# Performance work log

Measured on AMD Instinct MI355X. Metric: run time of the kernel, lower is better.

Reference implementation:

```python
import jax, jax.numpy as jnp
import numpy as np

B, H, I, E = 4096, 1024, 4096, 8
TOP_K = 2


def setup_inputs() -> dict:
    key = jax.random.key(0)
    ks = jax.random.split(key, 8)
    s = 0.02
    return {
        "x": jax.random.normal(ks[0], (B, H), jnp.float32),
        "noise": -jnp.log(-jnp.log(jax.random.uniform(ks[1], (B, E), jnp.float32) + 1e-20) + 1e-20),
        "Wr": jax.random.normal(ks[2], (H, E), jnp.float32) * s,
        "br": jnp.zeros((E,), jnp.float32),
        "W_in": jax.random.normal(ks[3], (E, H, 2 * I), jnp.float32) * s,
        "b_in": jnp.zeros((E, 2 * I), jnp.float32),
        "W_out": jax.random.normal(ks[4], (E, I, H), jnp.float32) * s,
        "b_out": jnp.zeros((E, H), jnp.float32),
    }


def reference(x, noise, Wr, br, W_in, b_in, W_out, b_out):
    # Router + Gumbel top-2 (temperature = 1.0)
    logits = x @ Wr + br                      # [B, E]
    y = logits + noise
    vals, idxs = jax.lax.top_k(y, TOP_K)      # [B, 2]
    w = jax.nn.softmax(vals, axis=-1)         # softmax over the 2 selected vals
    # Dense gate matrix: gates[b, e] = sum_k w[b,k] * (idxs[b,k] == e)
    onehot = (idxs[:, :, None] == jnp.arange(E)[None, None, :]).astype(x.dtype)  # [B,2,E]
    gates = jnp.einsum("bk,bke->be", w, onehot)                                   # [B,E]

    out = jnp.zeros_like(x)
    for e in range(E):  # small static expert loop
        h = x @ W_in[e] + b_in[e]             # [B, 2I]
        x1, x2 = jnp.split(h, 2, axis=-1)     # SwiGLU: chunk(2, dim=-1)
        a = x1 * jax.nn.sigmoid(x2)           # [B, I]
        o = a @ W_out[e] + b_out[e]           # [B, H]
        out = out + gates[:, e:e + 1] * o
    # dropout is identity in eval mode
    return out
```

## Files before the change

kernel.cpp:

```cpp
#include <hip/hip_runtime.h>

#define B_TOK 4096
#define HDIM 1024
#define IDIM 4096
#define NSLOT 8192
#define MAX_T128 72

using short8   = __attribute__((ext_vector_type(8))) short;
using bf16x8   = __attribute__((ext_vector_type(8))) __bf16;
using f32x4    = __attribute__((ext_vector_type(4))) float;
using int4v    = __attribute__((ext_vector_type(4))) int;
using ushort4v = __attribute__((ext_vector_type(4))) unsigned short;
using float4v  = __attribute__((ext_vector_type(4))) float;

#define MC_NT128   0
#define MC_E128    8
#define MC_M0128   80
#define MC_RW128   152
#define META_INTS  256

__device__ __forceinline__ unsigned short f2bf(float f) {
  unsigned u = __float_as_uint(f);
  u += 0x7FFFu + ((u >> 16) & 1u);
  return (unsigned short)(u >> 16);
}
__device__ __forceinline__ float bf2f(unsigned short h) {
  return __uint_as_float(((unsigned)h) << 16);
}
__device__ __forceinline__ f32x4 mfma_bf16(short8 a, short8 b, f32x4 c) {
  return __builtin_amdgcn_mfma_f32_16x16x32_bf16(
      __builtin_bit_cast(bf16x8, a), __builtin_bit_cast(bf16x8, b), c, 0, 0, 0);
}
__device__ __forceinline__ void gload16(const unsigned short* g, unsigned short* l) {
  __builtin_amdgcn_global_load_lds(
      (const __attribute__((address_space(1))) unsigned int*)g,
      (__attribute__((address_space(3))) unsigned int*)l, 16, 0, 0);
}

__global__ __launch_bounds__(256) void router_kernel(
    const float* __restrict__ x, const float* __restrict__ noise,
    const float* __restrict__ Wr, const float* __restrict__ br,
    int* __restrict__ idxmap, float* __restrict__ wmap) {
  int tok = blockIdx.x * 4 + (threadIdx.x >> 6);
  int l = threadIdx.x & 63;
  const float* xr = x + (size_t)tok * HDIM;
  float acc[8];
#pragma unroll
  for (int e = 0; e < 8; e++) acc[e] = 0.f;
  for (int hb = 0; hb < HDIM; hb += 256) {
    int h = hb + l * 4;
    float4v xv = *(const float4v*)(xr + h);
#pragma unroll
    for (int j = 0; j < 4; j++) {
      float4v w0 = *(const float4v*)(Wr + (size_t)(h + j) * 8);
      float4v w1 = *(const float4v*)(Wr + (size_t)(h + j) * 8 + 4);
      acc[0] += xv[j] * w0[0]; acc[1] += xv[j] * w0[1];
      acc[2] += xv[j] * w0[2]; acc[3] += xv[j] * w0[3];
      acc[4] += xv[j] * w1[0]; acc[5] += xv[j] * w1[1];
      acc[6] += xv[j] * w1[2]; acc[7] += xv[j] * w1[3];
    }
  }
#pragma unroll
  for (int off = 32; off > 0; off >>= 1) {
#pragma unroll
    for (int e = 0; e < 8; e++) acc[e] += __shfl_xor(acc[e], off, 64);
  }
  if (l == 0) {
    float y[8];
#pragma unroll
    for (int e = 0; e < 8; e++) y[e] = acc[e] + br[e] + noise[(size_t)tok * 8 + e];
    int e0 = 0;
#pragma unroll
    for (int e = 1; e < 8; e++) if (y[e] > y[e0]) e0 = e;
    int e1 = (e0 == 0) ? 1 : 0;
#pragma unroll
    for (int e = 0; e < 8; e++) if (e != e0 && y[e] > y[e1]) e1 = e;
    float w0 = 1.f / (1.f + __expf(y[e1] - y[e0]));
    idxmap[tok * 2] = e0; idxmap[tok * 2 + 1] = e1;
    wmap[tok * 2] = w0;   wmap[tok * 2 + 1] = 1.f - w0;
  }
}

__global__ __launch_bounds__(1024) void rank_kernel(
    const int* __restrict__ idxmap, int* __restrict__ slotmap,
    int* __restrict__ meta) {
  int tid = threadIdx.x, lane = tid & 63, wv = tid >> 6;
  __shared__ unsigned wtot[16][4];
  __shared__ unsigned woff[16][4];
  __shared__ unsigned offE[8];

  int es[8];
  unsigned p0 = 0, p1 = 0, p2 = 0, p3 = 0;
#pragma unroll
  for (int j = 0; j < 8; j++) {
    int e = idxmap[tid * 8 + j];
    es[j] = e;
    unsigned c = 1u << ((e & 1) * 16);
    if (e < 2) p0 += c; else if (e < 4) p1 += c;
    else if (e < 6) p2 += c; else p3 += c;
  }
  unsigned i0 = p0, i1 = p1, i2 = p2, i3 = p3;
#pragma unroll
  for (int d = 1; d < 64; d <<= 1) {
    unsigned t0 = __shfl_up(i0, d, 64), t1 = __shfl_up(i1, d, 64);
    unsigned t2 = __shfl_up(i2, d, 64), t3 = __shfl_up(i3, d, 64);
    if (lane >= d) { i0 += t0; i1 += t1; i2 += t2; i3 += t3; }
  }
  if (lane == 63) { wtot[wv][0] = i0; wtot[wv][1] = i1; wtot[wv][2] = i2; wtot[wv][3] = i3; }
  __syncthreads();
  if (wv == 0 && lane < 16) {
    unsigned a0 = wtot[lane][0], a1 = wtot[lane][1], a2 = wtot[lane][2], a3 = wtot[lane][3];
    unsigned s0 = a0, s1 = a1, s2 = a2, s3 = a3;
#pragma unroll
    for (int d = 1; d < 16; d <<= 1) {
      unsigned t0 = __shfl_up(s0, d, 64), t1 = __shfl_up(s1, d, 64);
      unsigned t2 = __shfl_up(s2, d, 64), t3 = __shfl_up(s3, d, 64);
      if (lane >= d) { s0 += t0; s1 += t1; s2 += t2; s3 += t3; }
    }
    woff[lane][0] = s0 - a0; woff[lane][1] = s1 - a1;
    woff[lane][2] = s2 - a2; woff[lane][3] = s3 - a3;
    if (lane == 15) {
      unsigned t[8];
      t[0] = s0 & 0xFFFF; t[1] = s0 >> 16; t[2] = s1 & 0xFFFF; t[3] = s1 >> 16;
      t[4] = s2 & 0xFFFF; t[5] = s2 >> 16; t[6] = s3 & 0xFFFF; t[7] = s3 >> 16;
      unsigned off = 0; int tc = 0;
      for (int e = 0; e < 8; e++) {
        offE[e] = off;
        for (unsigned i = 0; i < t[e]; i += 128) {
          meta[MC_E128 + tc] = e;
          meta[MC_M0128 + tc] = (int)(off + i);
          meta[MC_RW128 + tc] = (int)((t[e] - i < 128u) ? (t[e] - i) : 128u);
          tc++;
        }
        off += t[e];
      }
      meta[MC_NT128] = tc;
    }
  }
  __syncthreads();
  unsigned e0w = i0 - p0 + woff[wv][0];
  unsigned e1w = i1 - p1 + woff[wv][1];
  unsigned e2w = i2 - p2 + woff[wv][2];
  unsigned e3w = i3 - p3 + woff[wv][3];
#pragma unroll
  for (int j = 0; j < 8; j++) {
    int e = es[j];
    unsigned sh = (unsigned)(e & 1) * 16;
    unsigned c = 1u << sh, v;
    if (e < 2)      { v = (e0w >> sh) & 0xFFFF; e0w += c; }
    else if (e < 4) { v = (e1w >> sh) & 0xFFFF; e1w += c; }
    else if (e < 6) { v = (e2w >> sh) & 0xFFFF; e2w += c; }
    else            { v = (e3w >> sh) & 0xFFFF; e3w += c; }
    slotmap[tid * 8 + j] = (int)(offE[e] + v);
  }
}

__global__ __launch_bounds__(256) void place_kernel(
    const float* __restrict__ x, const int* __restrict__ slotmap,
    unsigned short* __restrict__ x_g) {
  int tok = blockIdx.x * 2 + (threadIdx.x >> 7);
  int h = (threadIdx.x & 127) * 8;
  const float* xr = x + (size_t)tok * HDIM + h;
  float4v v0 = *(const float4v*)xr;
  float4v v1 = *(const float4v*)(xr + 4);
  int4v p;
  p[0] = (int)((unsigned)f2bf(v0[0]) | ((unsigned)f2bf(v0[1]) << 16));
  p[1] = (int)((unsigned)f2bf(v0[2]) | ((unsigned)f2bf(v0[3]) << 16));
  p[2] = (int)((unsigned)f2bf(v1[0]) | ((unsigned)f2bf(v1[1]) << 16));
  p[3] = (int)((unsigned)f2bf(v1[2]) | ((unsigned)f2bf(v1[3]) << 16));
  int s0 = slotmap[tok * 2], s1 = slotmap[tok * 2 + 1];
  *(int4v*)(x_g + (size_t)s0 * HDIM + h) = p;
  *(int4v*)(x_g + (size_t)s1 * HDIM + h) = p;
}

__global__ __launch_bounds__(256) void prep_win_kernel(
    const float* __restrict__ W_in, unsigned short* __restrict__ Wt) {
  int e = blockIdx.z, k0 = blockIdx.y * 64, n0 = blockIdx.x * 64;
  __shared__ __align__(16) unsigned short T[64 * 72];
  int tid = threadIdx.x;
#pragma unroll
  for (int i = 0; i < 4; i++) {
    int q = i * 256 + tid;
    int kr = q >> 4, nc = (q & 15) * 4;
    float4v v = *(const float4v*)(W_in + ((size_t)e * 1024 + k0 + kr) * 8192 + n0 + nc);
#pragma unroll
    for (int j = 0; j < 4; j++) T[(nc + j) * 72 + kr] = f2bf(v[j]);
  }
  __syncthreads();
  int half = (n0 >= 4096) ? 1 : 0;
  int j0 = n0 - half * 4096;
  int J = j0 >> 6;
  unsigned short* ob = Wt + (((size_t)e * 64 + J) << 17);
#pragma unroll
  for (int i = 0; i < 2; i++) {
    int q = i * 256 + tid;
    int nr = q >> 3, kc = (q & 7) * 8;
    int pr = (nr >> 4) * 32 + half * 16 + (nr & 15);
    *(int4v*)(ob + (size_t)pr * 1024 + k0 + kc) = *(const int4v*)&T[nr * 72 + kc];
  }
}

__global__ __launch_bounds__(256) void prep_wout_kernel(
    const float* __restrict__ W_out, unsigned short* __restrict__ Wt) {
  int e = blockIdx.z, k0 = blockIdx.y * 64, n0 = blockIdx.x * 64;
  __shared__ __align__(16) unsigned short T[64 * 72];
  int tid = threadIdx.x;
#pragma unroll
  for (int i = 0; i < 4; i++) {
    int q = i * 256 + tid;
    int kr = q >> 4, nc = (q & 15) * 4;
    float4v v = *(const float4v*)(W_out + ((size_t)e * 4096 + k0 + kr) * 1024 + n0 + nc);
#pragma unroll
    for (int j = 0; j < 4; j++) T[(nc + j) * 72 + kr] = f2bf(v[j]);
  }
  __syncthreads();
  unsigned short* ob = Wt + ((size_t)e * 1024 + n0) * 4096;
#pragma unroll
  for (int i = 0; i < 2; i++) {
    int q = i * 256 + tid;
    int nr = q >> 3, kc = (q & 7) * 8;
    *(int4v*)(ob + (size_t)nr * 4096 + k0 + kc) = *(const int4v*)&T[nr * 72 + kc];
  }
}

__global__ __launch_bounds__(256, 4) void gemm1a_kernel(
    const unsigned short* __restrict__ x_g, const unsigned short* __restrict__ Wt,
    const float* __restrict__ b_in, unsigned short* __restrict__ a_buf,
    const int* __restrict__ meta) {
  int bid = blockIdx.x;
  int xcd = bid & 7, local = bid >> 3;
  int t = local >> 3;
  if (t >= meta[MC_NT128]) return;
  int J = xcd * 8 + (local & 7);
  int e = meta[MC_E128 + t];
  int m0 = meta[MC_M0128 + t];
  int rows = meta[MC_RW128 + t];
  const unsigned short* Wp = Wt + (((size_t)e * 64 + J) << 17);

  __shared__ __align__(16) unsigned short As[128 * 64];
  __shared__ __align__(16) unsigned short Bs[128 * 64];

  int tid = threadIdx.x, l = tid & 63, w = tid >> 6;
  int g = l >> 4, ln = l & 15, lr = l >> 3;
  int uc = (l & 7) ^ lr;
  int wm = w >> 1, wn = w & 1;

  const unsigned short* sA[4]; const unsigned short* sB[4]; int dO[4];
#pragma unroll
  for (int i = 0; i < 4; i++) {
    int c = w * 4 + i;
    int r = c * 8 + lr;
    int ra = r < rows ? r : rows - 1;
    sA[i] = x_g + (size_t)(m0 + ra) * HDIM + uc * 8;
    sB[i] = Wp + (size_t)r * 1024 + uc * 8;
    dO[i] = c * 512 + l * 8;
  }

  f32x4 acc[4][4];
#pragma unroll
  for (int mf = 0; mf < 4; mf++)
#pragma unroll
    for (int nf = 0; nf < 4; nf++) acc[mf][nf] = (f32x4){0.f, 0.f, 0.f, 0.f};

#pragma unroll 1
  for (int kt = 0; kt < 16; kt++) {
#pragma unroll
    for (int i = 0; i < 4; i++) gload16(sA[i] + kt * 64, &As[dO[i]]);
#pragma unroll
    for (int i = 0; i < 4; i++) gload16(sB[i] + kt * 64, &Bs[dO[i]]);
    __syncthreads();
#pragma unroll
    for (int ks = 0; ks < 2; ks++) {
      int u0 = (((ks * 4 + g) ^ (ln & 7)) << 3);
      short8 af[4], bfr[4];
#pragma unroll
      for (int mf = 0; mf < 4; mf++)
        af[mf] = *(const short8*)&As[(wm * 64 + mf * 16 + ln) * 64 + u0];
#pragma unroll
      for (int nf = 0; nf < 4; nf++)
        bfr[nf] = *(const short8*)&Bs[(wn * 64 + nf * 16 + ln) * 64 + u0];
#pragma unroll
      for (int mf = 0; mf < 4; mf++)
#pragma unroll
        for (int nf = 0; nf < 4; nf++)
          acc[mf][nf] = mfma_bf16(af[mf], bfr[nf], acc[mf][nf]);
    }
    __syncthreads();
  }
#pragma unroll
  for (int mf = 0; mf < 4; mf++) {
#pragma unroll
    for (int np = 0; np < 2; np++) {
      int j = J * 64 + wn * 32 + np * 16 + ln;
      float b1 = b_in[(size_t)e * 8192 + j];
      float b2 = b_in[(size_t)e * 8192 + 4096 + j];
#pragma unroll
      for (int r = 0; r < 4; r++) {
        int m = wm * 64 + mf * 16 + g * 4 + r;
        if (m < rows) {
          float h1 = acc[mf][np * 2][r] + b1;
          float h2 = acc[mf][np * 2 + 1][r] + b2;
          a_buf[(size_t)(m0 + m) * IDIM + j] = f2bf(h1 / (1.f + __expf(-h2)));
        }
      }
    }
  }
}

__global__ __launch_bounds__(256, 4) void gemm2a_kernel(
    const unsigned short* __restrict__ a_buf, const unsigned short* __restrict__ Wt,
    const float* __restrict__ b_out, unsigned short* __restrict__ buf2,
    const int* __restrict__ meta) {
  int bid = blockIdx.x;
  int xcd = bid & 7, local = bid >> 3;
  int t = local >> 1;
  if (t >= meta[MC_NT128]) return;
  int n0 = xcd * 128 + (local & 1) * 64;
  int e = meta[MC_E128 + t];
  int m0 = meta[MC_M0128 + t];
  int rows = meta[MC_RW128 + t];
  const unsigned short* Wp = Wt + ((size_t)e * 1024 + n0) * 4096;

  __shared__ __align__(16) unsigned short As[128 * 64];
  __shared__ __align__(16) unsigned short Bs[64 * 64];

  int tid = threadIdx.x, l = tid & 63, w = tid >> 6;
  int g = l >> 4, ln = l & 15, lr = l >> 3;
  int uc = (l & 7) ^ lr;
  int wm = w >> 1, wn = w & 1;

  const unsigned short* sA[4]; int dAo[4];
#pragma unroll
  for (int i = 0; i < 4; i++) {
    int c = w * 4 + i;
    int r = c * 8 + lr;
    int ra = r < rows ? r : rows - 1;
    sA[i] = a_buf + (size_t)(m0 + ra) * IDIM + uc * 8;
    dAo[i] = c * 512 + l * 8;
  }
  const unsigned short* sB[2]; int dBo[2];
#pragma unroll
  for (int i = 0; i < 2; i++) {
    int c = w * 2 + i;
    int r = c * 8 + lr;
    sB[i] = Wp + (size_t)r * 4096 + uc * 8;
    dBo[i] = c * 512 + l * 8;
  }

  f32x4 acc[4][2];
#pragma unroll
  for (int mf = 0; mf < 4; mf++)
#pragma unroll
    for (int nf = 0; nf < 2; nf++) acc[mf][nf] = (f32x4){0.f, 0.f, 0.f, 0.f};

#pragma unroll 1
  for (int kt = 0; kt < 64; kt++) {
#pragma unroll
    for (int i = 0; i < 4; i++) gload16(sA[i] + kt * 64, &As[dAo[i]]);
#pragma unroll
    for (int i = 0; i < 2; i++) gload16(sB[i] + kt * 64, &Bs[dBo[i]]);
    __syncthreads();
#pragma unroll
    for (int ks = 0; ks < 2; ks++) {
      int u0 = (((ks * 4 + g) ^ (ln & 7)) << 3);
      short8 af[4], bfr[2];
#pragma unroll
      for (int mf = 0; mf < 4; mf++)
        af[mf] = *(const short8*)&As[(wm * 64 + mf * 16 + ln) * 64 + u0];
#pragma unroll
      for (int nf = 0; nf < 2; nf++)
        bfr[nf] = *(const short8*)&Bs[(wn * 32 + nf * 16 + ln) * 64 + u0];
#pragma unroll
      for (int mf = 0; mf < 4; mf++)
#pragma unroll
        for (int nf = 0; nf < 2; nf++)
          acc[mf][nf] = mfma_bf16(af[mf], bfr[nf], acc[mf][nf]);
    }
    __syncthreads();
  }
#pragma unroll
  for (int mf = 0; mf < 4; mf++) {
#pragma unroll
    for (int nf = 0; nf < 2; nf++) {
      int col = n0 + wn * 32 + nf * 16 + ln;
      float bo = b_out[(size_t)e * 1024 + col];
#pragma unroll
      for (int r = 0; r < 4; r++) {
        int m = wm * 64 + mf * 16 + g * 4 + r;
        if (m < rows) {
          buf2[(size_t)(m0 + m) * HDIM + col] = f2bf(acc[mf][nf][r] + bo);
        }
      }
    }
  }
}

__global__ __launch_bounds__(256) void combine_kernel(
    const unsigned short* __restrict__ buf2, const int* __restrict__ slotmap,
    const float* __restrict__ wmap, float* __restrict__ out) {
  int i = blockIdx.x * 256 + threadIdx.x;
  int base = i * 4;
  int b = base >> 10, h = base & 1023;
  int s0 = slotmap[b * 2], s1 = slotmap[b * 2 + 1];
  float w0 = wmap[b * 2], w1 = wmap[b * 2 + 1];
  ushort4v c0 = *(const ushort4v*)(buf2 + (size_t)s0 * HDIM + h);
  ushort4v c1 = *(const ushort4v*)(buf2 + (size_t)s1 * HDIM + h);
  float4v o;
#pragma unroll
  for (int j = 0; j < 4; j++) o[j] = w0 * bf2f(c0[j]) + w1 * bf2f(c1[j]);
  *(float4v*)(out + base) = o;
}

extern "C" void kernel_launch(void* const* d_in, const int* in_sizes, int n_in,
                              void* d_out, int out_size, void* d_ws, size_t ws_size,
                              hipStream_t stream) {
  const float* x     = (const float*)d_in[0];
  const float* noise = (const float*)d_in[1];
  const float* Wr    = (const float*)d_in[2];
  const float* br    = (const float*)d_in[3];
  const float* W_in  = (const float*)d_in[4];
  const float* b_in  = (const float*)d_in[5];
  const float* W_out = (const float*)d_in[6];
  const float* b_out = (const float*)d_in[7];
  float* out = (float*)d_out;
  char* ws = (char*)d_ws;

  unsigned short* W_in_t  = (unsigned short*)ws;
  unsigned short* W_out_t = W_in_t;
  unsigned short* x_g     = (unsigned short*)(ws + 134217728);
  unsigned short* buf2    = x_g;
  unsigned short* a_buf   = (unsigned short*)(ws + 150994944);
  int* meta    = (int*)(ws + 218103808);
  int* idxmap  = meta + META_INTS;
  int* slotmap = idxmap + NSLOT;
  float* wmap  = (float*)(slotmap + NSLOT);

  hipLaunchKernelGGL(router_kernel, dim3(B_TOK / 4), dim3(256), 0, stream,
                     x, noise, Wr, br, idxmap, wmap);
  hipLaunchKernelGGL(rank_kernel, dim3(1), dim3(1024), 0, stream,
                     idxmap, slotmap, meta);
  hipLaunchKernelGGL(place_kernel, dim3(B_TOK / 2), dim3(256), 0, stream,
                     x, slotmap, x_g);
  hipLaunchKernelGGL(prep_win_kernel, dim3(128, 16, 8), dim3(256), 0, stream,
                     W_in, W_in_t);
  hipLaunchKernelGGL(gemm1a_kernel, dim3(8 * MAX_T128 * 8), dim3(256), 0, stream,
                     x_g, W_in_t, b_in, a_buf, meta);
  hipLaunchKernelGGL(prep_wout_kernel, dim3(16, 64, 8), dim3(256), 0, stream,
                     W_out, W_out_t);
  hipLaunchKernelGGL(gemm2a_kernel, dim3(8 * MAX_T128 * 2), dim3(256), 0, stream,
                     a_buf, W_out_t, b_out, buf2, meta);
  hipLaunchKernelGGL(combine_kernel, dim3((B_TOK * HDIM / 4) / 256), dim3(256), 0, stream,
                     buf2, slotmap, wmap, out);
}
```

Before: 451.1 us.

## Fuse weight prep into router and gemm1 launches, widen gemm2 N-tile

```diff
diff --git a/kernel.cpp b/kernel.cpp
--- a/kernel.cpp
+++ b/kernel.cpp
@@ -5,6 +5,7 @@
 #define IDIM 4096
 #define NSLOT 8192
 #define MAX_T128 72
+#define G1_BLOCKS (8 * MAX_T128 * 8)
 
 using short8   = __attribute__((ext_vector_type(8))) short;
 using bf16x8   = __attribute__((ext_vector_type(8))) __bf16;
@@ -37,47 +38,99 @@
       (__attribute__((address_space(3))) unsigned int*)l, 16, 0, 0);
 }
 
-__global__ __launch_bounds__(256) void router_kernel(
+__device__ __forceinline__ void prep_wout_body(
+    const float* __restrict__ W_out, unsigned short* __restrict__ Wt,
+    int bx, int by, int e, unsigned short* T, int tid) {
+  int k0 = by * 64, n0 = bx * 64;
+#pragma unroll
+  for (int i = 0; i < 4; i++) {
+    int q = i * 256 + tid;
+    int kr = q >> 4, nc = (q & 15) * 4;
+    float4v v = *(const float4v*)(W_out + ((size_t)e * 4096 + k0 + kr) * 1024 + n0 + nc);
+#pragma unroll
+    for (int j = 0; j < 4; j++) T[(nc + j) * 72 + kr] = f2bf(v[j]);
+  }
+  __syncthreads();
+  unsigned short* ob = Wt + ((size_t)e * 1024 + n0) * 4096;
+#pragma unroll
+  for (int i = 0; i < 2; i++) {
+    int q = i * 256 + tid;
+    int nr = q >> 3, kc = (q & 7) * 8;
+    *(int4v*)(ob + (size_t)nr * 4096 + k0 + kc) = *(const int4v*)&T[nr * 72 + kc];
+  }
+}
+
+__global__ __launch_bounds__(256) void fused_pre_kernel(
     const float* __restrict__ x, const float* __restrict__ noise,
     const float* __restrict__ Wr, const float* __restrict__ br,
-    int* __restrict__ idxmap, float* __restrict__ wmap) {
-  int tok = blockIdx.x * 4 + (threadIdx.x >> 6);
-  int l = threadIdx.x & 63;
-  const float* xr = x + (size_t)tok * HDIM;
-  float acc[8];
-#pragma unroll
-  for (int e = 0; e < 8; e++) acc[e] = 0.f;
-  for (int hb = 0; hb < HDIM; hb += 256) {
-    int h = hb + l * 4;
-    float4v xv = *(const float4v*)(xr + h);
-#pragma unroll
-    for (int j = 0; j < 4; j++) {
-      float4v w0 = *(const float4v*)(Wr + (size_t)(h + j) * 8);
-      float4v w1 = *(const float4v*)(Wr + (size_t)(h + j) * 8 + 4);
-      acc[0] += xv[j] * w0[0]; acc[1] += xv[j] * w0[1];
-      acc[2] += xv[j] * w0[2]; acc[3] += xv[j] * w0[3];
-      acc[4] += xv[j] * w1[0]; acc[5] += xv[j] * w1[1];
-      acc[6] += xv[j] * w1[2]; acc[7] += xv[j] * w1[3];
-    }
-  }
-#pragma unroll
-  for (int off = 32; off > 0; off >>= 1) {
-#pragma unroll
-    for (int e = 0; e < 8; e++) acc[e] += __shfl_xor(acc[e], off, 64);
-  }
-  if (l == 0) {
-    float y[8];
-#pragma unroll
-    for (int e = 0; e < 8; e++) y[e] = acc[e] + br[e] + noise[(size_t)tok * 8 + e];
-    int e0 = 0;
-#pragma unroll
-    for (int e = 1; e < 8; e++) if (y[e] > y[e0]) e0 = e;
-    int e1 = (e0 == 0) ? 1 : 0;
-#pragma unroll
-    for (int e = 0; e < 8; e++) if (e != e0 && y[e] > y[e1]) e1 = e;
-    float w0 = 1.f / (1.f + __expf(y[e1] - y[e0]));
-    idxmap[tok * 2] = e0; idxmap[tok * 2 + 1] = e1;
-    wmap[tok * 2] = w0;   wmap[tok * 2 + 1] = 1.f - w0;
+    int* __restrict__ idxmap, float* __restrict__ wmap,
+    const float* __restrict__ W_in, unsigned short* __restrict__ Wt) {
+  __shared__ __align__(16) unsigned short T[64 * 72];
+  int bid = blockIdx.x;
+  int tid = threadIdx.x;
+  if (bid < 1024) {
+    int tok = bid * 4 + (tid >> 6);
+    int l = tid & 63;
+    const float* xr = x + (size_t)tok * HDIM;
+    float acc[8];
+#pragma unroll
+    for (int e = 0; e < 8; e++) acc[e] = 0.f;
+    for (int hb = 0; hb < HDIM; hb += 256) {
+      int h = hb + l * 4;
+      float4v xv = *(const float4v*)(xr + h);
+#pragma unroll
+      for (int j = 0; j < 4; j++) {
+        float4v w0 = *(const float4v*)(Wr + (size_t)(h + j) * 8);
+        float4v w1 = *(const float4v*)(Wr + (size_t)(h + j) * 8 + 4);
+        acc[0] += xv[j] * w0[0]; acc[1] += xv[j] * w0[1];
+        acc[2] += xv[j] * w0[2]; acc[3] += xv[j] * w0[3];
+        acc[4] += xv[j] * w1[0]; acc[5] += xv[j] * w1[1];
+        acc[6] += xv[j] * w1[2]; acc[7] += xv[j] * w1[3];
+      }
+    }
+#pragma unroll
+    for (int off = 32; off > 0; off >>= 1) {
+#pragma unroll
+      for (int e = 0; e < 8; e++) acc[e] += __shfl_xor(acc[e], off, 64);
+    }
+    if (l == 0) {
+      float y[8];
+#pragma unroll
+      for (int e = 0; e < 8; e++) y[e] = acc[e] + br[e] + noise[(size_t)tok * 8 + e];
+      int e0 = 0;
+#pragma unroll
+      for (int e = 1; e < 8; e++) if (y[e] > y[e0]) e0 = e;
+      int e1 = (e0 == 0) ? 1 : 0;
+#pragma unroll
+      for (int e = 0; e < 8; e++) if (e != e0 && y[e] > y[e1]) e1 = e;
+      float w0 = 1.f / (1.f + __expf(y[e1] - y[e0]));
+      idxmap[tok * 2] = e0; idxmap[tok * 2 + 1] = e1;
+      wmap[tok * 2] = w0;   wmap[tok * 2 + 1] = 1.f - w0;
+    }
+    return;
+  }
+  int pid = bid - 1024;
+  int e = pid >> 11, rem = pid & 2047;
+  int k0 = (rem >> 7) * 64, n0 = (rem & 127) * 64;
+#pragma unroll
+  for (int i = 0; i < 4; i++) {
+    int q = i * 256 + tid;
+    int kr = q >> 4, nc = (q & 15) * 4;
+    float4v v = *(const float4v*)(W_in + ((size_t)e * 1024 + k0 + kr) * 8192 + n0 + nc);
+#pragma unroll
+    for (int j = 0; j < 4; j++) T[(nc + j) * 72 + kr] = f2bf(v[j]);
+  }
+  __syncthreads();
+  int half = (n0 >= 4096) ? 1 : 0;
+  int j0 = n0 - half * 4096;
+  int J = j0 >> 6;
+  unsigned short* ob = Wt + (((size_t)e * 64 + J) << 17);
+#pragma unroll
+  for (int i = 0; i < 2; i++) {
+    int q = i * 256 + tid;
+    int nr = q >> 3, kc = (q & 7) * 8;
+    int pr = (nr >> 4) * 32 + half * 16 + (nr & 15);
+    *(int4v*)(ob + (size_t)pr * 1024 + k0 + kc) = *(const int4v*)&T[nr * 72 + kc];
   }
 }
 
@@ -173,61 +226,26 @@
   *(int4v*)(x_g + (size_t)s1 * HDIM + h) = p;
 }
 
-__global__ __launch_bounds__(256) void prep_win_kernel(
-    const float* __restrict__ W_in, unsigned short* __restrict__ Wt) {
-  int e = blockIdx.z, k0 = blockIdx.y * 64, n0 = blockIdx.x * 64;
-  __shared__ __align__(16) unsigned short T[64 * 72];
-  int tid = threadIdx.x;
-#pragma unroll
-  for (int i = 0; i < 4; i++) {
-    int q = i * 256 + tid;
-    int kr = q >> 4, nc = (q & 15) * 4;
-    float4v v = *(const float4v*)(W_in + ((size_t)e * 1024 + k0 + kr) * 8192 + n0 + nc);
-#pragma unroll
-    for (int j = 0; j < 4; j++) T[(nc + j) * 72 + kr] = f2bf(v[j]);
-  }
-  __syncthreads();
-  int half = (n0 >= 4096) ? 1 : 0;
-  int j0 = n0 - half * 4096;
-  int J = j0 >> 6;
-  unsigned short* ob = Wt + (((size_t)e * 64 + J) << 17);
-#pragma unroll
-  for (int i = 0; i < 2; i++) {
-    int q = i * 256 + tid;
-    int nr = q >> 3, kc = (q & 7) * 8;
-    int pr = (nr >> 4) * 32 + half * 16 + (nr & 15);
-    *(int4v*)(ob + (size_t)pr * 1024 + k0 + kc) = *(const int4v*)&T[nr * 72 + kc];
-  }
-}
-
 __global__ __launch_bounds__(256) void prep_wout_kernel(
     const float* __restrict__ W_out, unsigned short* __restrict__ Wt) {
-  int e = blockIdx.z, k0 = blockIdx.y * 64, n0 = blockIdx.x * 64;
   __shared__ __align__(16) unsigned short T[64 * 72];
-  int tid = threadIdx.x;
-#pragma unroll
-  for (int i = 0; i < 4; i++) {
-    int q = i * 256 + tid;
-    int kr = q >> 4, nc = (q & 15) * 4;
-    float4v v = *(const float4v*)(W_out + ((size_t)e * 4096 + k0 + kr) * 1024 + n0 + nc);
-#pragma unroll
-    for (int j = 0; j < 4; j++) T[(nc + j) * 72 + kr] = f2bf(v[j]);
-  }
-  __syncthreads();
-  unsigned short* ob = Wt + ((size_t)e * 1024 + n0) * 4096;
-#pragma unroll
-  for (int i = 0; i < 2; i++) {
-    int q = i * 256 + tid;
-    int nr = q >> 3, kc = (q & 7) * 8;
-    *(int4v*)(ob + (size_t)nr * 4096 + k0 + kc) = *(const int4v*)&T[nr * 72 + kc];
-  }
+  prep_wout_body(W_out, Wt, blockIdx.x, blockIdx.y, blockIdx.z, T, threadIdx.x);
 }
 
 __global__ __launch_bounds__(256, 4) void gemm1a_kernel(
     const unsigned short* __restrict__ x_g, const unsigned short* __restrict__ Wt,
     const float* __restrict__ b_in, unsigned short* __restrict__ a_buf,
-    const int* __restrict__ meta) {
+    const int* __restrict__ meta,
+    const float* __restrict__ W_out, unsigned short* __restrict__ Wot) {
+  __shared__ __align__(16) unsigned short As[128 * 64];
+  __shared__ __align__(16) unsigned short Bs[128 * 64];
   int bid = blockIdx.x;
+  if (bid >= G1_BLOCKS) {
+    int pid = bid - G1_BLOCKS;
+    int e = pid >> 10, rem = pid & 1023;
+    prep_wout_body(W_out, Wot, rem & 15, rem >> 4, e, As, threadIdx.x);
+    return;
+  }
   int xcd = bid & 7, local = bid >> 3;
   int t = local >> 3;
   if (t >= meta[MC_NT128]) return;
@@ -237,9 +255,6 @@
   int rows = meta[MC_RW128 + t];
   const unsigned short* Wp = Wt + (((size_t)e * 64 + J) << 17);
 
-  __shared__ __align__(16) unsigned short As[128 * 64];
-  __shared__ __align__(16) unsigned short Bs[128 * 64];
-
   int tid = threadIdx.x, l = tid & 63, w = tid >> 6;
   int g = l >> 4, ln = l & 15, lr = l >> 3;
   int uc = (l & 7) ^ lr;
@@ -312,68 +327,61 @@
     const float* __restrict__ b_out, unsigned short* __restrict__ buf2,
     const int* __restrict__ meta) {
   int bid = blockIdx.x;
-  int xcd = bid & 7, local = bid >> 3;
-  int t = local >> 1;
+  int xcd = bid & 7;
+  int t = bid >> 3;
   if (t >= meta[MC_NT128]) return;
-  int n0 = xcd * 128 + (local & 1) * 64;
+  int n0 = xcd * 128;
   int e = meta[MC_E128 + t];
   int m0 = meta[MC_M0128 + t];
   int rows = meta[MC_RW128 + t];
   const unsigned short* Wp = Wt + ((size_t)e * 1024 + n0) * 4096;
 
   __shared__ __align__(16) unsigned short As[128 * 64];
-  __shared__ __align__(16) unsigned short Bs[64 * 64];
+  __shared__ __align__(16) unsigned short Bs[128 * 64];
 
   int tid = threadIdx.x, l = tid & 63, w = tid >> 6;
   int g = l >> 4, ln = l & 15, lr = l >> 3;
   int uc = (l & 7) ^ lr;
   int wm = w >> 1, wn = w & 1;
 
-  const unsigned short* sA[4]; int dAo[4];
+  const unsigned short* sA[4]; const unsigned short* sB[4]; int dO[4];
 #pragma unroll
   for (int i = 0; i < 4; i++) {
     int c = w * 4 + i;
     int r = c * 8 + lr;
     int ra = r < rows ? r : rows - 1;
     sA[i] = a_buf + (size_t)(m0 + ra) * IDIM + uc * 8;
-    dAo[i] = c * 512 + l * 8;
-  }
-  const unsigned short* sB[2]; int dBo[2];
-#pragma unroll
-  for (int i = 0; i < 2; i++) {
-    int c = w * 2 + i;
-    int r = c * 8 + lr;
     sB[i] = Wp + (size_t)r * 4096 + uc * 8;
-    dBo[i] = c * 512 + l * 8;
-  }
-
-  f32x4 acc[4][2];
+    dO[i] = c * 512 + l * 8;
+  }
+
+  f32x4 acc[4][4];
 #pragma unroll
   for (int mf = 0; mf < 4; mf++)
 #pragma unroll
-    for (int nf = 0; nf < 2; nf++) acc[mf][nf] = (f32x4){0.f, 0.f, 0.f, 0.f};
+    for (int nf = 0; nf < 4; nf++) acc[mf][nf] = (f32x4){0.f, 0.f, 0.f, 0.f};
 
 #pragma unroll 1
   for (int kt = 0; kt < 64; kt++) {
 #pragma unroll
-    for (int i = 0; i < 4; i++) gload16(sA[i] + kt * 64, &As[dAo[i]]);
-#pragma unroll
-    for (int i = 0; i < 2; i++) gload16(sB[i] + kt * 64, &Bs[dBo[i]]);
+    for (int i = 0; i < 4; i++) gload16(sA[i] + kt * 64, &As[dO[i]]);
+#pragma unroll
+    for (int i = 0; i < 4; i++) gload16(sB[i] + kt * 64, &Bs[dO[i]]);
     __syncthreads();
 #pragma unroll
     for (int ks = 0; ks < 2; ks++) {
       int u0 = (((ks * 4 + g) ^ (ln & 7)) << 3);
-      short8 af[4], bfr[2];
+      short8 af[4], bfr[4];
 #pragma unroll
       for (int mf = 0; mf < 4; mf++)
         af[mf] = *(const short8*)&As[(wm * 64 + mf * 16 + ln) * 64 + u0];
 #pragma unroll
-      for (int nf = 0; nf < 2; nf++)
-        bfr[nf] = *(const short8*)&Bs[(wn * 32 + nf * 16 + ln) * 64 + u0];
+      for (int nf = 0; nf < 4; nf++)
+        bfr[nf] = *(const short8*)&Bs[(wn * 64 + nf * 16 + ln) * 64 + u0];
 #pragma unroll
       for (int mf = 0; mf < 4; mf++)
 #pragma unroll
-        for (int nf = 0; nf < 2; nf++)
+        for (int nf = 0; nf < 4; nf++)
           acc[mf][nf] = mfma_bf16(af[mf], bfr[nf], acc[mf][nf]);
     }
     __syncthreads();
@@ -381,8 +389,8 @@
 #pragma unroll
   for (int mf = 0; mf < 4; mf++) {
 #pragma unroll
-    for (int nf = 0; nf < 2; nf++) {
-      int col = n0 + wn * 32 + nf * 16 + ln;
+    for (int nf = 0; nf < 4; nf++) {
+      int col = n0 + wn * 64 + nf * 16 + ln;
       float bo = b_out[(size_t)e * 1024 + col];
 #pragma unroll
       for (int r = 0; r < 4; r++) {
@@ -425,29 +433,34 @@
   float* out = (float*)d_out;
   char* ws = (char*)d_ws;
 
+  const size_t NEED_B = 285343744ULL;
+  bool big = (ws_size >= NEED_B);
+
   unsigned short* W_in_t  = (unsigned short*)ws;
-  unsigned short* W_out_t = W_in_t;
   unsigned short* x_g     = (unsigned short*)(ws + 134217728);
   unsigned short* buf2    = x_g;
   unsigned short* a_buf   = (unsigned short*)(ws + 150994944);
-  int* meta    = (int*)(ws + 218103808);
+  unsigned short* W_out_t = big ? (unsigned short*)(ws + 218103808)
+                                : W_in_t;
+  int* meta    = (int*)(ws + (big ? 285212672 : 218103808));
   int* idxmap  = meta + META_INTS;
   int* slotmap = idxmap + NSLOT;
   float* wmap  = (float*)(slotmap + NSLOT);
 
-  hipLaunchKernelGGL(router_kernel, dim3(B_TOK / 4), dim3(256), 0, stream,
-                     x, noise, Wr, br, idxmap, wmap);
+  hipLaunchKernelGGL(fused_pre_kernel, dim3(1024 + 16384), dim3(256), 0, stream,
+                     x, noise, Wr, br, idxmap, wmap, W_in, W_in_t);
   hipLaunchKernelGGL(rank_kernel, dim3(1), dim3(1024), 0, stream,
                      idxmap, slotmap, meta);
   hipLaunchKernelGGL(place_kernel, dim3(B_TOK / 2), dim3(256), 0, stream,
                      x, slotmap, x_g);
-  hipLaunchKernelGGL(prep_win_kernel, dim3(128, 16, 8), dim3(256), 0, stream,
-                     W_in, W_in_t);
-  hipLaunchKernelGGL(gemm1a_kernel, dim3(8 * MAX_T128 * 8), dim3(256), 0, stream,
-                     x_g, W_in_t, b_in, a_buf, meta);
-  hipLaunchKernelGGL(prep_wout_kernel, dim3(16, 64, 8), dim3(256), 0, stream,
-                     W_out, W_out_t);
-  hipLaunchKernelGGL(gemm2a_kernel, dim3(8 * MAX_T128 * 2), dim3(256), 0, stream,
+  hipLaunchKernelGGL(gemm1a_kernel,
+                     dim3(big ? (G1_BLOCKS + 8192) : G1_BLOCKS), dim3(256), 0, stream,
+                     x_g, W_in_t, b_in, a_buf, meta, W_out, W_out_t);
+  if (!big) {
+    hipLaunchKernelGGL(prep_wout_kernel, dim3(16, 64, 8), dim3(256), 0, stream,
+                       W_out, W_out_t);
+  }
+  hipLaunchKernelGGL(gemm2a_kernel, dim3(8 * MAX_T128), dim3(256), 0, stream,
                      a_buf, W_out_t, b_out, buf2, meta);
   hipLaunchKernelGGL(combine_kernel, dim3((B_TOK * HDIM / 4) / 256), dim3(256), 0, stream,
                      buf2, slotmap, wmap, out);
```

New measurement: 404.4 us. 10.4% less time.
